# Kernel optimization log

Measured on AMD Instinct MI355X. Metric: run time of the kernel, lower is better.

Reference implementation:

```python
import math
import jax, jax.numpy as jnp
import numpy as np

V = 50257; T = 1024; D = 1024; H = 16; L = 4; DS = 3; B = 2
DH = D // H; DF = 4 * D
PEN = 1.0; EW = 0.01; FW = 0.1; RW = 0.01


def setup_inputs() -> dict:
    key = jax.random.key(0)
    ks = jax.random.split(key, 12)
    p = lambda k, s: jax.random.normal(k, s, jnp.float32) * 0.02
    return dict(
        idx=jax.random.randint(ks[0], (B, T), 0, V),
        targets=jax.random.randint(ks[1], (B, T), 0, V),
        emb=p(ks[2], (V, D)),                      # tied token emb / lm_head
        pos_emb=p(ks[3], (T, D)),
        positions=jax.random.normal(ks[4], (L, T, DS)) * 0.3,
        ln1_g=jnp.ones((L, D)), ln1_b=jnp.zeros((L, D)),
        ln2_g=jnp.ones((L, D)), ln2_b=jnp.zeros((L, D)),
        lnf_g=jnp.ones((D,)), lnf_b=jnp.zeros((D,)),
        qkv_w=p(ks[5], (L, D, 3 * D)),             # stored [in,out] (= torch W.T)
        proj_w=p(ks[6], (L, D, D)),
        w1=p(ks[7], (L, D, DF)), b1=jnp.zeros((L, DF)),
        w2=p(ks[8], (L, DF, D)), b2=jnp.zeros((L, D)),
    )


def _ln(x, g, b, eps=1e-5):
    m = x.mean(-1, keepdims=True)
    v = ((x - m) ** 2).mean(-1, keepdims=True)
    return (x - m) * jax.lax.rsqrt(v + eps) * g + b


def _safe_dists(pos):
    # pairwise L2 distance with zero (not nan) gradient on the diagonal
    diff = pos[:, None, :] - pos[None, :, :]      # [T,T,DS]
    sq = (diff ** 2).sum(-1)
    return jnp.where(sq > 0, jnp.sqrt(jnp.where(sq > 0, sq, 1.0)), 0.0)


def reference(idx, targets, emb, pos_emb, positions, ln1_g, ln1_b, ln2_g, ln2_b,
              lnf_g, lnf_b, qkv_w, proj_w, w1, b1, w2, b2):
    x = emb[idx] + pos_emb[None, :, :]            # [B,T,D]; dropout = identity (eval)
    causal = jnp.triu(jnp.ones((T, T), bool), 1)
    offd = ~jnp.eye(T, dtype=bool)
    scale = 1.0 / math.sqrt(DH)
    tde = jnp.float32(0.0); tfe = jnp.float32(0.0); tre = jnp.float32(0.0)
    all_w = []; all_d = []
    for l in range(L):
        h = _ln(x, ln1_g[l], ln1_b[l])
        q, k, v = jnp.split(h @ qkv_w[l], 3, axis=-1)
        rs = lambda t: t.reshape(B, T, H, DH).transpose(0, 2, 1, 3)  # [B,H,T,DH]
        q, k, v = rs(q), rs(k), rs(v)
        logits_a = jnp.einsum('bhid,bhjd->bhij', q, k) * scale
        dists = _safe_dists(positions[l])                       # [T,T]
        logits_a = logits_a - PEN * dists
        logits_a = jnp.where(causal, -jnp.inf, logits_a)
        w = jax.nn.softmax(logits_a, axis=-1)                   # [B,H,T,T]
        tde = tde + (w * dists).sum(-1).mean()
        tfe = tfe + (-(w * jnp.log(w + 1e-9)).sum(-1)).mean()
        tre = tre + jnp.where(offd, 1.0 / (dists + 1e-4), 0.0).sum() / (T * T - T)
        out = jnp.einsum('bhij,bhjd->bhid', w, v).transpose(0, 2, 1, 3).reshape(B, T, D)
        x = x + out @ proj_w[l]
        h2 = _ln(x, ln2_g[l], ln2_b[l])
        x = x + (jax.nn.gelu(h2 @ w1[l] + b1[l], approximate=False) @ w2[l] + b2[l])
        all_w.append(jax.lax.stop_gradient(w))
        all_d.append(jax.lax.stop_gradient(dists))
    logits = _ln(x, lnf_g, lnf_b) @ emb.T                       # tied lm_head
    logp = jax.nn.log_softmax(logits, axis=-1)
    ce = -jnp.take_along_axis(logp, targets[..., None], axis=-1).mean()
    loss = ce + EW * tde + FW * tfe + RW * tre
    return (logits, loss, tde, tfe, tre, tuple(all_w), tuple(all_d))
```

## Files before the change

kernel.cpp:

```cpp
#include <hip/hip_runtime.h>
#include <hip/hip_bf16.h>
#include <cmath>

#define TT 1024
#define DD 1024
#define HH 16
#define LL 4
#define BB 2
#define DHH 64
#define DFF 4096
#define VV 50257

typedef float floatx4 __attribute__((ext_vector_type(4)));
typedef __bf16 bf16x8 __attribute__((ext_vector_type(8)));

typedef unsigned int u32;
typedef __attribute__((address_space(1))) const u32 gu32;
typedef __attribute__((address_space(3))) u32 lu32;

__device__ __forceinline__ void gload16(const unsigned short* g, unsigned short* l) {
  __builtin_amdgcn_global_load_lds((gu32*)g, (lu32*)l, 16, 0, 0);
}

__device__ __forceinline__ unsigned short f2bf(float f) {
  unsigned u = __float_as_uint(f);
  u += 0x7fffu + ((u >> 16) & 1u);
  return (unsigned short)(u >> 16);
}

__device__ __forceinline__ float wave_sum(float v) {
#pragma unroll
  for (int off = 1; off < 64; off <<= 1) v += __shfl_xor(v, off);
  return v;
}
__device__ __forceinline__ float wave_max(float v) {
#pragma unroll
  for (int off = 1; off < 64; off <<= 1) v = fmaxf(v, __shfl_xor(v, off));
  return v;
}

#define EPI_F32 0
#define EPI_QKV 1
#define EPI_ATT 2
#define EPI_RES 3
#define EPI_GELU 4
#define EPI_RESBIAS 5
#define EPI_LSE 6

struct GemmArgs {
  const unsigned short* A;
  const unsigned short* B;
  long aBatch, bBatch, cBatch;
  int M, N, K, ldc;
  float* outF;
  unsigned short* q;
  unsigned short* kk;
  unsigned short* vt;
  unsigned short* outB;
  const float* bias;
  float* res;
  float2* lsePart;
  int pn;
  int kchunk;
};

template <int EPI>
__global__ __launch_bounds__(256) void gemm_kernel(GemmArgs ga) {
  __shared__ __align__(16) unsigned short As[128 * 32];
  __shared__ __align__(16) unsigned short Bs[128 * 32];
  const int tid = threadIdx.x;
  const int bm = blockIdx.y * 128;
  const int bn = blockIdx.x * 128;
  const int z = blockIdx.z;
  const unsigned short* A = ga.A + (long)z * ga.aBatch;
  const unsigned short* Bp = ga.B + (long)z * ga.bBatch;
  const int K = ga.K, N = ga.N;

  int kbeg = 0, kend = K;
  if constexpr (EPI == EPI_RES || EPI == EPI_RESBIAS) {
    kbeg = z * ga.kchunk; kend = kbeg + ga.kchunk;
  }

  floatx4 acc[4][4];
#pragma unroll
  for (int i = 0; i < 4; ++i)
#pragma unroll
    for (int j = 0; j < 4; ++j) acc[i][j] = (floatx4){0.f, 0.f, 0.f, 0.f};

  const int lane = tid & 63, wave = tid >> 6;
  const int wm = (wave & 1) * 64, wn = (wave >> 1) * 64;
  const int fr = lane & 15, quad = lane >> 4;
  const int srow = tid >> 2;
  const int sc8 = (tid & 3) * 8;

  unsigned short* lA0 = &As[wave * 512];
  unsigned short* lA1 = &As[2048 + wave * 512];
  unsigned short* lB0 = &Bs[wave * 512];
  unsigned short* lB1 = &Bs[2048 + wave * 512];

  for (int k0 = kbeg; k0 < kend; k0 += 32) {
    const long ra = (long)(bm + srow) * K + (k0 + sc8);
    const long rb = (long)(bn + srow) * K + (k0 + sc8);
    gload16(A + ra, lA0);
    gload16(A + ra + 64L * K, lA1);
    gload16(Bp + rb, lB0);
    gload16(Bp + rb + 64L * K, lB1);
    __syncthreads();
    bf16x8 af[4], bfr[4];
#pragma unroll
    for (int i = 0; i < 4; ++i) af[i] = *(const bf16x8*)(&As[(wm + i * 16 + fr) * 32 + quad * 8]);
#pragma unroll
    for (int j = 0; j < 4; ++j) bfr[j] = *(const bf16x8*)(&Bs[(wn + j * 16 + fr) * 32 + quad * 8]);
#pragma unroll
    for (int i = 0; i < 4; ++i)
#pragma unroll
      for (int j = 0; j < 4; ++j)
        acc[i][j] = __builtin_amdgcn_mfma_f32_16x16x32_bf16(af[i], bfr[j], acc[i][j], 0, 0, 0);
    __syncthreads();
  }

  if constexpr (EPI == EPI_LSE) {
    float2* sm = (float2*)As;
#pragma unroll
    for (int i = 0; i < 4; ++i) {
#pragma unroll
      for (int r = 0; r < 4; ++r) {
        const int m = bm + wm + i * 16 + quad * 4 + r;
        float mx = -INFINITY, ss = 0.f;
#pragma unroll
        for (int j = 0; j < 4; ++j) {
          const int n = bn + wn + j * 16 + fr;
          const float val = acc[i][j][r];
          float v;
          if (n < N) { ga.outF[(long)m * ga.ldc + n] = val; v = val; }
          else v = -INFINITY;
          if (v > mx) { ss = ss * __expf(mx - v) + 1.f; mx = v; }
          else ss += __expf(v - mx);
        }
#pragma unroll
        for (int off = 1; off < 16; off <<= 1) {
          const float mo = __shfl_xor(mx, off), so = __shfl_xor(ss, off);
          const float M = fmaxf(mx, mo);
          ss = ss * __expf(mx - M) + so * __expf(mo - M);
          mx = M;
        }
        if (fr == 0) {
          const int rl = wm + i * 16 + quad * 4 + r;
          sm[rl * 2 + (wave >> 1)] = make_float2(mx, ss);
        }
      }
    }
    __syncthreads();
    if (tid < 128) {
      const float2 a = sm[tid * 2], b = sm[tid * 2 + 1];
      const float M = fmaxf(a.x, b.x);
      const float S = a.y * __expf(a.x - M) + b.y * __expf(b.x - M);
      ga.lsePart[(long)(bm + tid) * ga.pn + blockIdx.x] = make_float2(M, S);
    }
  } else {
#pragma unroll
    for (int i = 0; i < 4; ++i) {
#pragma unroll
      for (int j = 0; j < 4; ++j) {
        const int n = bn + wn + j * 16 + fr;
#pragma unroll
        for (int r = 0; r < 4; ++r) {
          const int m = bm + wm + i * 16 + quad * 4 + r;
          const float val = acc[i][j][r];
          if constexpr (EPI == EPI_F32) {
            if (n < N) ga.outF[(long)z * ga.cBatch + (long)m * ga.ldc + n] = val;
          }
          if constexpr (EPI == EPI_QKV) {
            const int b = m >> 10, t = m & 1023;
            const int sec = n >> 10, col = n & 1023;
            const int hd = col >> 6, dh = col & 63;
            const unsigned short bv = f2bf(val);
            if (sec == 0)      ga.q [((long)(b * HH + hd) * TT + t) * DHH + dh] = bv;
            else if (sec == 1) ga.kk[((long)(b * HH + hd) * TT + t) * DHH + dh] = bv;
            else               ga.vt[((long)(b * HH + hd) * DHH + dh) * TT + t] = bv;
          }
          if constexpr (EPI == EPI_ATT) {
            if (n < 64) {
              const int b = z >> 4, hd = z & 15;
              ga.outB[((long)(b * TT + m)) * DD + hd * DHH + n] = f2bf(val);
            }
          }
          if constexpr (EPI == EPI_RES) {
            atomicAdd(&ga.res[(long)m * DD + n], val);
          }
          if constexpr (EPI == EPI_GELU) {
            const float xx = val + ga.bias[n];
            const float gl = 0.5f * xx * (1.f + erff(xx * 0.7071067811865475f));
            ga.outB[(long)m * DFF + n] = f2bf(gl);
          }
          if constexpr (EPI == EPI_RESBIAS) {
            const float badd = (z == 0) ? ga.bias[n] : 0.f;
            atomicAdd(&ga.res[(long)m * DD + n], val + badd);
          }
        }
      }
    }
  }
}

__global__ __launch_bounds__(256) void transpose_bf16_kernel(const float* __restrict__ src,
    unsigned short* __restrict__ dst, int R, int C) {
  __shared__ float tile[32][33];
  const int c0 = blockIdx.x * 32, r0 = blockIdx.y * 32;
  const int tx = threadIdx.x & 31, ty = threadIdx.x >> 5;
#pragma unroll
  for (int rr = ty; rr < 32; rr += 8)
    tile[rr][tx] = src[(long)(r0 + rr) * C + (c0 + tx)];
  __syncthreads();
#pragma unroll
  for (int rr = ty; rr < 32; rr += 8)
    dst[(long)(c0 + rr) * R + (r0 + tx)] = f2bf(tile[tx][rr]);
}

__global__ __launch_bounds__(256) void convert_bf16_kernel(const float* __restrict__ in,
    unsigned short* __restrict__ out) {
  const long i = (long)blockIdx.x * 256 + threadIdx.x;
  const float4 v = ((const float4*)in)[i];
  ushort4 o;
  o.x = f2bf(v.x); o.y = f2bf(v.y); o.z = f2bf(v.z); o.w = f2bf(v.w);
  ((ushort4*)out)[i] = o;
}

__global__ __launch_bounds__(256) void embed_kernel(const int* __restrict__ idx,
    const float* __restrict__ emb, const float* __restrict__ pos, float* __restrict__ x) {
  const int bt = blockIdx.x;
  const int t = bt & (TT - 1);
  const int tok = idx[bt];
  const float4 e = ((const float4*)(emb + (long)tok * DD))[threadIdx.x];
  const float4 p = ((const float4*)(pos + (long)t * DD))[threadIdx.x];
  float4 o; o.x = e.x + p.x; o.y = e.y + p.y; o.z = e.z + p.z; o.w = e.w + p.w;
  ((float4*)(x + (long)bt * DD))[threadIdx.x] = o;
}

__global__ __launch_bounds__(256) void ln_kernel(const float* __restrict__ x,
    const float* __restrict__ g, const float* __restrict__ b, unsigned short* __restrict__ out) {
  const int row = blockIdx.x;
  const float4 v = ((const float4*)(x + (long)row * DD))[threadIdx.x];
  float s = v.x + v.y + v.z + v.w;
  float s2 = v.x * v.x + v.y * v.y + v.z * v.z + v.w * v.w;
  s = wave_sum(s); s2 = wave_sum(s2);
  __shared__ float ps[4], ps2[4];
  const int wv = threadIdx.x >> 6, lane = threadIdx.x & 63;
  if (lane == 0) { ps[wv] = s; ps2[wv] = s2; }
  __syncthreads();
  s = ps[0] + ps[1] + ps[2] + ps[3];
  s2 = ps2[0] + ps2[1] + ps2[2] + ps2[3];
  const float mean = s * (1.f / DD);
  const float var = s2 * (1.f / DD) - mean * mean;
  const float rs = rsqrtf(var + 1e-5f);
  const float4 gv = ((const float4*)g)[threadIdx.x];
  const float4 bv = ((const float4*)b)[threadIdx.x];
  ushort4 o;
  o.x = f2bf((v.x - mean) * rs * gv.x + bv.x);
  o.y = f2bf((v.y - mean) * rs * gv.y + bv.y);
  o.z = f2bf((v.z - mean) * rs * gv.z + bv.z);
  o.w = f2bf((v.w - mean) * rs * gv.w + bv.w);
  ((ushort4*)(out + (long)row * DD))[threadIdx.x] = o;
}

__global__ __launch_bounds__(256) void dists_kernel(const float* __restrict__ pos,
    float* __restrict__ dout, float* __restrict__ tre_acc) {
  const int i = blockIdx.x;
  const float px = pos[i * 3], py = pos[i * 3 + 1], pz = pos[i * 3 + 2];
  float rsum = 0.f;
#pragma unroll
  for (int c = 0; c < 4; ++c) {
    const int j = c * 256 + threadIdx.x;
    const float dx = px - pos[j * 3];
    const float dy = py - pos[j * 3 + 1];
    const float dz = pz - pos[j * 3 + 2];
    const float sq = dx * dx + dy * dy + dz * dz;
    const float d = sq > 0.f ? sqrtf(sq) : 0.f;
    dout[(long)i * TT + j] = d;
    if (j != i) rsum += 1.f / (d + 1e-4f);
  }
  rsum = wave_sum(rsum);
  __shared__ float ps[4];
  const int wv = threadIdx.x >> 6, lane = threadIdx.x & 63;
  if (lane == 0) ps[wv] = rsum;
  __syncthreads();
  if (threadIdx.x == 0) atomicAdd(tre_acc, ps[0] + ps[1] + ps[2] + ps[3]);
}

__global__ __launch_bounds__(256) void softmax_kernel(float* __restrict__ S,
    const float* __restrict__ dists, unsigned short* __restrict__ wb,
    float2* __restrict__ partials) {
  const long row = blockIdx.x;
  const int i = (int)(row & (TT - 1));
  float* Sr = S + row * TT;
  const float* dr = dists + (long)i * TT;
  const int j0 = threadIdx.x * 4;

  const float4 dv = ((const float4*)dr)[threadIdx.x];
  const float4 sv = ((const float4*)Sr)[threadIdx.x];
  float d[4] = {dv.x, dv.y, dv.z, dv.w};
  float sa[4] = {sv.x, sv.y, sv.z, sv.w};
  float l[4];
  float mx = -INFINITY;
#pragma unroll
  for (int c = 0; c < 4; ++c) {
    float v = sa[c] * 0.125f - d[c];
    if (j0 + c > i) v = -INFINITY;
    l[c] = v;
    mx = fmaxf(mx, v);
  }
  mx = wave_max(mx);
  __shared__ float rmax[4], rsm[4], rwd[4], rent[4];
  const int wv = threadIdx.x >> 6, lane = threadIdx.x & 63;
  if (lane == 0) rmax[wv] = mx;
  __syncthreads();
  mx = fmaxf(fmaxf(rmax[0], rmax[1]), fmaxf(rmax[2], rmax[3]));
  float e[4], sum = 0.f;
#pragma unroll
  for (int c = 0; c < 4; ++c) { e[c] = __expf(l[c] - mx); sum += e[c]; }
  sum = wave_sum(sum);
  if (lane == 0) rsm[wv] = sum;
  __syncthreads();
  sum = rsm[0] + rsm[1] + rsm[2] + rsm[3];
  const float inv = 1.f / sum;
  float4 wo;
  ushort4 bo;
  const float w0 = e[0] * inv, w1 = e[1] * inv, w2 = e[2] * inv, w3 = e[3] * inv;
  wo.x = w0; wo.y = w1; wo.z = w2; wo.w = w3;
  bo.x = f2bf(w0); bo.y = f2bf(w1); bo.z = f2bf(w2); bo.w = f2bf(w3);
  float wd = w0 * d[0] + w1 * d[1] + w2 * d[2] + w3 * d[3];
  float ent = -(w0 * __logf(w0 + 1e-9f) + w1 * __logf(w1 + 1e-9f)
        + w2 * __logf(w2 + 1e-9f) + w3 * __logf(w3 + 1e-9f));
  ((float4*)Sr)[threadIdx.x] = wo;
  ((ushort4*)(wb + row * TT))[threadIdx.x] = bo;
  wd = wave_sum(wd); ent = wave_sum(ent);
  if (lane == 0) { rwd[wv] = wd; rent[wv] = ent; }
  __syncthreads();
  if (threadIdx.x == 0) {
    partials[row] = make_float2(rwd[0] + rwd[1] + rwd[2] + rwd[3],
                                rent[0] + rent[1] + rent[2] + rent[3]);
  }
}

__global__ __launch_bounds__(256) void reduce_partials_kernel(const float2* __restrict__ p,
    int n, float* __restrict__ tde_acc, float* __restrict__ tfe_acc) {
  float wd = 0.f, ent = 0.f;
  for (int i = blockIdx.x * 256 + threadIdx.x; i < n; i += gridDim.x * 256) {
    const float2 v = p[i];
    wd += v.x; ent += v.y;
  }
  wd = wave_sum(wd); ent = wave_sum(ent);
  __shared__ float pw[4], pe[4];
  const int wv = threadIdx.x >> 6, lane = threadIdx.x & 63;
  if (lane == 0) { pw[wv] = wd; pe[wv] = ent; }
  __syncthreads();
  if (threadIdx.x == 0) {
    atomicAdd(tde_acc, pw[0] + pw[1] + pw[2] + pw[3]);
    atomicAdd(tfe_acc, pe[0] + pe[1] + pe[2] + pe[3]);
  }
}

__global__ __launch_bounds__(256) void ce_reduce_kernel(const float2* __restrict__ part,
    const float* __restrict__ logits, const int* __restrict__ targets,
    float* __restrict__ ce_acc, int pn) {
  const int row = blockIdx.x;
  const float2* pr = part + (long)row * pn;
  float m = -INFINITY, s = 0.f;
  for (int i = threadIdx.x; i < pn; i += 256) {
    const float2 v = pr[i];
    const float M = fmaxf(m, v.x);
    s = s * __expf(m - M) + v.y * __expf(v.x - M);
    m = M;
  }
#pragma unroll
  for (int off = 1; off < 64; off <<= 1) {
    const float mo = __shfl_xor(m, off), so = __shfl_xor(s, off);
    const float M = fmaxf(m, mo);
    s = s * __expf(m - M) + so * __expf(mo - M);
    m = M;
  }
  __shared__ float pm[4], psv[4];
  const int wv = threadIdx.x >> 6, lane = threadIdx.x & 63;
  if (lane == 0) { pm[wv] = m; psv[wv] = s; }
  __syncthreads();
  if (threadIdx.x == 0) {
    const float M = fmaxf(fmaxf(pm[0], pm[1]), fmaxf(pm[2], pm[3]));
    const float S = psv[0] * __expf(pm[0] - M) + psv[1] * __expf(pm[1] - M)
                  + psv[2] * __expf(pm[2] - M) + psv[3] * __expf(pm[3] - M);
    atomicAdd(ce_acc, M + logf(S) - logits[(long)row * VV + targets[row]]);
  }
}

__global__ void zero_acc_kernel(float* p) { if (threadIdx.x < 4) p[threadIdx.x] = 0.f; }

__global__ void finalize_kernel(const float* __restrict__ acc, float* __restrict__ o) {
  if (threadIdx.x == 0) {
    const float tde = acc[0] * (1.f / 32768.f);
    const float tfe = acc[1] * (1.f / 32768.f);
    const float tre = acc[2] * (1.f / 1047552.f);
    const float ce = acc[3] * (1.f / 2048.f);
    o[0] = ce + 0.01f * tde + 0.1f * tfe + 0.01f * tre;
    o[1] = tde; o[2] = tfe; o[3] = tre;
  }
}

extern "C" void kernel_launch(void* const* d_in, const int* in_sizes, int n_in,
                              void* d_out, int out_size, void* d_ws, size_t ws_size,
                              hipStream_t stream) {
  const int* idx = (const int*)d_in[0];
  const int* targets = (const int*)d_in[1];
  const float* emb = (const float*)d_in[2];
  const float* pos_emb = (const float*)d_in[3];
  const float* positions = (const float*)d_in[4];
  const float* ln1_g = (const float*)d_in[5];
  const float* ln1_b = (const float*)d_in[6];
  const float* ln2_g = (const float*)d_in[7];
  const float* ln2_b = (const float*)d_in[8];
  const float* lnf_g = (const float*)d_in[9];
  const float* lnf_b = (const float*)d_in[10];
  const float* qkv_w = (const float*)d_in[11];
  const float* proj_w = (const float*)d_in[12];
  const float* w1 = (const float*)d_in[13];
  const float* b1 = (const float*)d_in[14];
  const float* w2 = (const float*)d_in[15];
  const float* b2 = (const float*)d_in[16];

  float* out = (float*)d_out;
  char* ws = (char*)d_ws;

  const long LOGITS_N = (long)BB * TT * VV;
  const long SCAL_OFF = LOGITS_N;
  const long ALLW_OFF = LOGITS_N + 4;
  const long ALLW_STRIDE = (long)BB * HH * TT * TT;
  const long ALLD_OFF = ALLW_OFF + 4 * ALLW_STRIDE;
  const long ALLD_STRIDE = (long)TT * TT;

  unsigned short* wt_qkv  = (unsigned short*)(ws);
  unsigned short* wt_proj = (unsigned short*)(ws + 25165824L);
  unsigned short* wt_w1   = (unsigned short*)(ws + 33554432L);
  unsigned short* wt_w2   = (unsigned short*)(ws + 67108864L);
  unsigned short* emb_bf  = (unsigned short*)(ws + 100663296L);
  float*          x       = (float*)(ws + 203589632L);
  unsigned short* h_bf    = (unsigned short*)(ws + 211978240L);
  unsigned short* q_bf    = (unsigned short*)(ws + 216172544L);
  unsigned short* k_bf    = (unsigned short*)(ws + 220366848L);
  unsigned short* vt_bf   = (unsigned short*)(ws + 224561152L);
  unsigned short* attb_bf = (unsigned short*)(ws + 228755456L);
  unsigned short* g_bf    = (unsigned short*)(ws + 232949760L);
  unsigned short* w_bf    = (unsigned short*)(ws + 249726976L);
  float*          accs    = (float*)(ws + 316835840L);

  float2* smpart = (float2*)attb_bf;
  float2* lsepart = (float2*)wt_qkv;
  const int LSE_PN = (VV + 127) / 128;

  const dim3 blk(256);

  for (int l = 0; l < LL; ++l) {
    transpose_bf16_kernel<<<dim3(3 * DD / 32, DD / 32), blk, 0, stream>>>(
        qkv_w + (long)l * DD * 3 * DD, wt_qkv + (long)l * 3 * DD * DD, DD, 3 * DD);
    transpose_bf16_kernel<<<dim3(DD / 32, DD / 32), blk, 0, stream>>>(
        proj_w + (long)l * DD * DD, wt_proj + (long)l * DD * DD, DD, DD);
    transpose_bf16_kernel<<<dim3(DFF / 32, DD / 32), blk, 0, stream>>>(
        w1 + (long)l * DD * DFF, wt_w1 + (long)l * DFF * DD, DD, DFF);
    transpose_bf16_kernel<<<dim3(DD / 32, DFF / 32), blk, 0, stream>>>(
        w2 + (long)l * DFF * DD, wt_w2 + (long)l * DD * DFF, DFF, DD);
  }
  convert_bf16_kernel<<<VV, blk, 0, stream>>>(emb, emb_bf);

  embed_kernel<<<BB * TT, blk, 0, stream>>>(idx, emb, pos_emb, x);
  zero_acc_kernel<<<1, 64, 0, stream>>>(accs);

  for (int l = 0; l < LL; ++l) {
    float* allw_l = out + ALLW_OFF + (long)l * ALLW_STRIDE;
    float* alld_l = out + ALLD_OFF + (long)l * ALLD_STRIDE;

    dists_kernel<<<TT, blk, 0, stream>>>(positions + (long)l * TT * 3, alld_l, accs + 2);
    ln_kernel<<<BB * TT, blk, 0, stream>>>(x, ln1_g + l * DD, ln1_b + l * DD, h_bf);

    { GemmArgs ga = {}; ga.A = h_bf; ga.B = wt_qkv + (long)l * 3 * DD * DD;
      ga.M = BB * TT; ga.N = 3 * DD; ga.K = DD;
      ga.q = q_bf; ga.kk = k_bf; ga.vt = vt_bf;
      gemm_kernel<EPI_QKV><<<dim3(24, 16, 1), blk, 0, stream>>>(ga); }

    { GemmArgs ga = {}; ga.A = q_bf; ga.B = k_bf;
      ga.aBatch = (long)TT * DHH; ga.bBatch = (long)TT * DHH;
      ga.M = TT; ga.N = TT; ga.K = DHH;
      ga.outF = allw_l; ga.ldc = TT; ga.cBatch = (long)TT * TT;
      gemm_kernel<EPI_F32><<<dim3(8, 8, BB * HH), blk, 0, stream>>>(ga); }

    softmax_kernel<<<BB * HH * TT, blk, 0, stream>>>(allw_l, alld_l, w_bf, smpart);
    reduce_partials_kernel<<<64, blk, 0, stream>>>(smpart, BB * HH * TT, accs + 0, accs + 1);

    { GemmArgs ga = {}; ga.A = w_bf; ga.B = vt_bf;
      ga.aBatch = (long)TT * TT; ga.bBatch = (long)DHH * TT;
      ga.M = TT; ga.N = DHH; ga.K = TT;
      ga.outB = attb_bf;
      gemm_kernel<EPI_ATT><<<dim3(1, 8, BB * HH), blk, 0, stream>>>(ga); }

    { GemmArgs ga = {}; ga.A = attb_bf; ga.B = wt_proj + (long)l * DD * DD;
      ga.M = BB * TT; ga.N = DD; ga.K = DD;
      ga.res = x; ga.kchunk = DD / 2;
      gemm_kernel<EPI_RES><<<dim3(8, 16, 2), blk, 0, stream>>>(ga); }

    ln_kernel<<<BB * TT, blk, 0, stream>>>(x, ln2_g + l * DD, ln2_b + l * DD, h_bf);

    { GemmArgs ga = {}; ga.A = h_bf; ga.B = wt_w1 + (long)l * DFF * DD;
      ga.M = BB * TT; ga.N = DFF; ga.K = DD;
      ga.bias = b1 + (long)l * DFF; ga.outB = g_bf;
      gemm_kernel<EPI_GELU><<<dim3(32, 16, 1), blk, 0, stream>>>(ga); }

    { GemmArgs ga = {}; ga.A = g_bf; ga.B = wt_w2 + (long)l * DD * DFF;
      ga.M = BB * TT; ga.N = DD; ga.K = DFF;
      ga.bias = b2 + (long)l * DD; ga.res = x; ga.kchunk = DFF / 4;
      gemm_kernel<EPI_RESBIAS><<<dim3(8, 16, 4), blk, 0, stream>>>(ga); }
  }

  ln_kernel<<<BB * TT, blk, 0, stream>>>(x, lnf_g, lnf_b, h_bf);

  { GemmArgs ga = {}; ga.A = h_bf; ga.B = emb_bf;
    ga.M = BB * TT; ga.N = VV; ga.K = DD;
    ga.outF = out; ga.ldc = VV; ga.cBatch = 0;
    ga.lsePart = lsepart; ga.pn = LSE_PN;
    gemm_kernel<EPI_LSE><<<dim3(LSE_PN, 16, 1), blk, 0, stream>>>(ga); }

  ce_reduce_kernel<<<BB * TT, blk, 0, stream>>>(lsepart, out, targets, accs + 3, LSE_PN);
  finalize_kernel<<<1, 64, 0, stream>>>(accs, out + SCAL_OFF);
}
```

Baseline: 2.860 ms.

## Store causal attention scores in bf16, skip masked tiles, and fuse residual adds into LayerNorm

The QK^T GEMM now launches only the lower-triangular 128x128 tiles, mapping a linear block index to (row, col) with a sqrt. It writes bf16 scores into the w_bf buffer, which the softmax reads and overwrites in place while still writing the fp32 weights output. The proj and FFN2 split-K GEMMs write fp32 partial buffers instead of doing atomicAdd into x. A new LN kernel then sums x, both partials and the bias before normalizing. This removes fp32 score traffic, masked-tile compute and atomic contention, at the cost of bf16 rounding of the logits and an extra partial-buffer read/write.

```diff
diff --git a/kernel.cpp b/kernel.cpp
--- a/kernel.cpp
+++ b/kernel.cpp
@@ -27,6 +27,9 @@
   u += 0x7fffu + ((u >> 16) & 1u);
   return (unsigned short)(u >> 16);
 }
+__device__ __forceinline__ float bf2f(unsigned short u) {
+  return __uint_as_float(((unsigned)u) << 16);
+}
 
 __device__ __forceinline__ float wave_sum(float v) {
 #pragma unroll
@@ -42,10 +45,9 @@
 #define EPI_F32 0
 #define EPI_QKV 1
 #define EPI_ATT 2
-#define EPI_RES 3
-#define EPI_GELU 4
-#define EPI_RESBIAS 5
-#define EPI_LSE 6
+#define EPI_GELU 3
+#define EPI_LSE 4
+#define EPI_SBF 5
 
 struct GemmArgs {
   const unsigned short* A;
@@ -58,7 +60,6 @@
   unsigned short* vt;
   unsigned short* outB;
   const float* bias;
-  float* res;
   float2* lsePart;
   int pn;
   int kchunk;
@@ -69,17 +70,24 @@
   __shared__ __align__(16) unsigned short As[128 * 32];
   __shared__ __align__(16) unsigned short Bs[128 * 32];
   const int tid = threadIdx.x;
-  const int bm = blockIdx.y * 128;
-  const int bn = blockIdx.x * 128;
+  int bm, bn;
+  if constexpr (EPI == EPI_SBF) {
+    const int xb = blockIdx.x;
+    int r = (int)((sqrtf(8.f * xb + 1.f) - 1.f) * 0.5f);
+    if ((r * (r + 1)) / 2 > xb) --r;
+    else if (((r + 1) * (r + 2)) / 2 <= xb) ++r;
+    const int c = xb - (r * (r + 1)) / 2;
+    bm = r * 128; bn = c * 128;
+  } else {
+    bm = blockIdx.y * 128; bn = blockIdx.x * 128;
+  }
   const int z = blockIdx.z;
   const unsigned short* A = ga.A + (long)z * ga.aBatch;
   const unsigned short* Bp = ga.B + (long)z * ga.bBatch;
   const int K = ga.K, N = ga.N;
 
   int kbeg = 0, kend = K;
-  if constexpr (EPI == EPI_RES || EPI == EPI_RESBIAS) {
-    kbeg = z * ga.kchunk; kend = kbeg + ga.kchunk;
-  }
+  if (ga.kchunk) { kbeg = z * ga.kchunk; kend = kbeg + ga.kchunk; }
 
   floatx4 acc[4][4];
 #pragma unroll
@@ -170,6 +178,9 @@
           if constexpr (EPI == EPI_F32) {
             if (n < N) ga.outF[(long)z * ga.cBatch + (long)m * ga.ldc + n] = val;
           }
+          if constexpr (EPI == EPI_SBF) {
+            ga.outB[(long)z * TT * TT + (long)m * TT + n] = f2bf(val);
+          }
           if constexpr (EPI == EPI_QKV) {
             const int b = m >> 10, t = m & 1023;
             const int sec = n >> 10, col = n & 1023;
@@ -185,17 +196,10 @@
               ga.outB[((long)(b * TT + m)) * DD + hd * DHH + n] = f2bf(val);
             }
           }
-          if constexpr (EPI == EPI_RES) {
-            atomicAdd(&ga.res[(long)m * DD + n], val);
-          }
           if constexpr (EPI == EPI_GELU) {
             const float xx = val + ga.bias[n];
             const float gl = 0.5f * xx * (1.f + erff(xx * 0.7071067811865475f));
             ga.outB[(long)m * DFF + n] = f2bf(gl);
-          }
-          if constexpr (EPI == EPI_RESBIAS) {
-            const float badd = (z == 0) ? ga.bias[n] : 0.f;
-            atomicAdd(&ga.res[(long)m * DD + n], val + badd);
           }
         }
       }
@@ -263,6 +267,43 @@
   ((ushort4*)(out + (long)row * DD))[threadIdx.x] = o;
 }
 
+__global__ __launch_bounds__(256) void ln_fuse_kernel(float* __restrict__ x,
+    const float* __restrict__ p0, const float* __restrict__ p1,
+    const float* __restrict__ bias,
+    const float* __restrict__ g, const float* __restrict__ b,
+    unsigned short* __restrict__ out) {
+  const int row = blockIdx.x;
+  float4 v = ((const float4*)(x + (long)row * DD))[threadIdx.x];
+  const float4 a0 = ((const float4*)(p0 + (long)row * DD))[threadIdx.x];
+  const float4 a1 = ((const float4*)(p1 + (long)row * DD))[threadIdx.x];
+  v.x += a0.x + a1.x; v.y += a0.y + a1.y; v.z += a0.z + a1.z; v.w += a0.w + a1.w;
+  if (bias) {
+    const float4 bb = ((const float4*)bias)[threadIdx.x];
+    v.x += bb.x; v.y += bb.y; v.z += bb.z; v.w += bb.w;
+  }
+  ((float4*)(x + (long)row * DD))[threadIdx.x] = v;
+  float s = v.x + v.y + v.z + v.w;
+  float s2 = v.x * v.x + v.y * v.y + v.z * v.z + v.w * v.w;
+  s = wave_sum(s); s2 = wave_sum(s2);
+  __shared__ float ps[4], ps2[4];
+  const int wv = threadIdx.x >> 6, lane = threadIdx.x & 63;
+  if (lane == 0) { ps[wv] = s; ps2[wv] = s2; }
+  __syncthreads();
+  s = ps[0] + ps[1] + ps[2] + ps[3];
+  s2 = ps2[0] + ps2[1] + ps2[2] + ps2[3];
+  const float mean = s * (1.f / DD);
+  const float var = s2 * (1.f / DD) - mean * mean;
+  const float rs = rsqrtf(var + 1e-5f);
+  const float4 gv = ((const float4*)g)[threadIdx.x];
+  const float4 bv = ((const float4*)b)[threadIdx.x];
+  ushort4 o;
+  o.x = f2bf((v.x - mean) * rs * gv.x + bv.x);
+  o.y = f2bf((v.y - mean) * rs * gv.y + bv.y);
+  o.z = f2bf((v.z - mean) * rs * gv.z + bv.z);
+  o.w = f2bf((v.w - mean) * rs * gv.w + bv.w);
+  ((ushort4*)(out + (long)row * DD))[threadIdx.x] = o;
+}
+
 __global__ __launch_bounds__(256) void dists_kernel(const float* __restrict__ pos,
     float* __restrict__ dout, float* __restrict__ tre_acc) {
   const int i = blockIdx.x;
@@ -287,19 +328,19 @@
   if (threadIdx.x == 0) atomicAdd(tre_acc, ps[0] + ps[1] + ps[2] + ps[3]);
 }
 
-__global__ __launch_bounds__(256) void softmax_kernel(float* __restrict__ S,
-    const float* __restrict__ dists, unsigned short* __restrict__ wb,
+__global__ __launch_bounds__(256) void softmax_kernel(unsigned short* __restrict__ wb,
+    const float* __restrict__ dists, float* __restrict__ W,
     float2* __restrict__ partials) {
   const long row = blockIdx.x;
   const int i = (int)(row & (TT - 1));
-  float* Sr = S + row * TT;
+  unsigned short* sr = wb + row * TT;
   const float* dr = dists + (long)i * TT;
   const int j0 = threadIdx.x * 4;
 
   const float4 dv = ((const float4*)dr)[threadIdx.x];
-  const float4 sv = ((const float4*)Sr)[threadIdx.x];
+  const ushort4 su = ((const ushort4*)sr)[threadIdx.x];
   float d[4] = {dv.x, dv.y, dv.z, dv.w};
-  float sa[4] = {sv.x, sv.y, sv.z, sv.w};
+  float sa[4] = {bf2f(su.x), bf2f(su.y), bf2f(su.z), bf2f(su.w)};
   float l[4];
   float mx = -INFINITY;
 #pragma unroll
@@ -331,8 +372,8 @@
   float wd = w0 * d[0] + w1 * d[1] + w2 * d[2] + w3 * d[3];
   float ent = -(w0 * __logf(w0 + 1e-9f) + w1 * __logf(w1 + 1e-9f)
         + w2 * __logf(w2 + 1e-9f) + w3 * __logf(w3 + 1e-9f));
-  ((float4*)Sr)[threadIdx.x] = wo;
-  ((ushort4*)(wb + row * TT))[threadIdx.x] = bo;
+  ((float4*)(W + row * TT))[threadIdx.x] = wo;
+  ((ushort4*)sr)[threadIdx.x] = bo;
   wd = wave_sum(wd); ent = wave_sum(ent);
   if (lane == 0) { rwd[wv] = wd; rent[wv] = ent; }
   __syncthreads();
@@ -452,6 +493,9 @@
 
   float2* smpart = (float2*)attb_bf;
   float2* lsepart = (float2*)wt_qkv;
+  float* pp = (float*)w_bf;
+  float* fp = (float*)w_bf + 2L * 2048 * DD;
+  const long RES_PART = (long)2048 * DD;
   const int LSE_PN = (VV + 127) / 128;
 
   const dim3 blk(256);
@@ -476,7 +520,11 @@
     float* alld_l = out + ALLD_OFF + (long)l * ALLD_STRIDE;
 
     dists_kernel<<<TT, blk, 0, stream>>>(positions + (long)l * TT * 3, alld_l, accs + 2);
-    ln_kernel<<<BB * TT, blk, 0, stream>>>(x, ln1_g + l * DD, ln1_b + l * DD, h_bf);
+    if (l == 0)
+      ln_kernel<<<BB * TT, blk, 0, stream>>>(x, ln1_g, ln1_b, h_bf);
+    else
+      ln_fuse_kernel<<<BB * TT, blk, 0, stream>>>(x, fp, fp + RES_PART,
+          b2 + (long)(l - 1) * DD, ln1_g + l * DD, ln1_b + l * DD, h_bf);
 
     { GemmArgs ga = {}; ga.A = h_bf; ga.B = wt_qkv + (long)l * 3 * DD * DD;
       ga.M = BB * TT; ga.N = 3 * DD; ga.K = DD;
@@ -486,10 +534,10 @@
     { GemmArgs ga = {}; ga.A = q_bf; ga.B = k_bf;
       ga.aBatch = (long)TT * DHH; ga.bBatch = (long)TT * DHH;
       ga.M = TT; ga.N = TT; ga.K = DHH;
-      ga.outF = allw_l; ga.ldc = TT; ga.cBatch = (long)TT * TT;
-      gemm_kernel<EPI_F32><<<dim3(8, 8, BB * HH), blk, 0, stream>>>(ga); }
-
-    softmax_kernel<<<BB * HH * TT, blk, 0, stream>>>(allw_l, alld_l, w_bf, smpart);
+      ga.outB = w_bf;
+      gemm_kernel<EPI_SBF><<<dim3(36, 1, BB * HH), blk, 0, stream>>>(ga); }
+
+    softmax_kernel<<<BB * HH * TT, blk, 0, stream>>>(w_bf, alld_l, allw_l, smpart);
     reduce_partials_kernel<<<64, blk, 0, stream>>>(smpart, BB * HH * TT, accs + 0, accs + 1);
 
     { GemmArgs ga = {}; ga.A = w_bf; ga.B = vt_bf;
@@ -499,11 +547,12 @@
       gemm_kernel<EPI_ATT><<<dim3(1, 8, BB * HH), blk, 0, stream>>>(ga); }
 
     { GemmArgs ga = {}; ga.A = attb_bf; ga.B = wt_proj + (long)l * DD * DD;
-      ga.M = BB * TT; ga.N = DD; ga.K = DD;
-      ga.res = x; ga.kchunk = DD / 2;
-      gemm_kernel<EPI_RES><<<dim3(8, 16, 2), blk, 0, stream>>>(ga); }
-
-    ln_kernel<<<BB * TT, blk, 0, stream>>>(x, ln2_g + l * DD, ln2_b + l * DD, h_bf);
+      ga.M = BB * TT; ga.N = DD; ga.K = DD; ga.ldc = DD;
+      ga.outF = pp; ga.cBatch = RES_PART; ga.kchunk = DD / 2;
+      gemm_kernel<EPI_F32><<<dim3(8, 16, 2), blk, 0, stream>>>(ga); }
+
+    ln_fuse_kernel<<<BB * TT, blk, 0, stream>>>(x, pp, pp + RES_PART,
+        nullptr, ln2_g + l * DD, ln2_b + l * DD, h_bf);
 
     { GemmArgs ga = {}; ga.A = h_bf; ga.B = wt_w1 + (long)l * DFF * DD;
       ga.M = BB * TT; ga.N = DFF; ga.K = DD;
@@ -511,12 +560,13 @@
       gemm_kernel<EPI_GELU><<<dim3(32, 16, 1), blk, 0, stream>>>(ga); }
 
     { GemmArgs ga = {}; ga.A = g_bf; ga.B = wt_w2 + (long)l * DD * DFF;
-      ga.M = BB * TT; ga.N = DD; ga.K = DFF;
-      ga.bias = b2 + (long)l * DD; ga.res = x; ga.kchunk = DFF / 4;
-      gemm_kernel<EPI_RESBIAS><<<dim3(8, 16, 4), blk, 0, stream>>>(ga); }
-  }
-
-  ln_kernel<<<BB * TT, blk, 0, stream>>>(x, lnf_g, lnf_b, h_bf);
+      ga.M = BB * TT; ga.N = DD; ga.K = DFF; ga.ldc = DD;
+      ga.outF = fp; ga.cBatch = RES_PART; ga.kchunk = DFF / 2;
+      gemm_kernel<EPI_F32><<<dim3(8, 16, 2), blk, 0, stream>>>(ga); }
+  }
+
+  ln_fuse_kernel<<<BB * TT, blk, 0, stream>>>(x, fp, fp + RES_PART,
+      b2 + (long)(LL - 1) * DD, lnf_g, lnf_b, h_bf);
 
   { GemmArgs ga = {}; ga.A = h_bf; ga.B = emb_bf;
     ga.M = BB * TT; ga.N = VV; ga.K = DD;
```

Result: faster. 2.741 ms (-4.2%).
